# Optimization experiments

Measured on AMD Instinct MI355X. Metric: run time of the kernel, lower is better.

Reference implementation:

```python
import jax, jax.numpy as jnp
import numpy as np

H, C = 8, 16           # heads, per-head channels
NEG_SLOPE = 0.2        # PyG GATConv leaky_relu slope
N_NODES, N_EDGES, F_IN, N_GRAPHS = 50000, 600000, 64, 500


def setup_inputs() -> dict:
    key = jax.random.key(0)
    ks = jax.random.split(key, 24)
    s = 0.1  # weight init scale
    inp = {
        "x": jax.random.normal(ks[0], (N_NODES, F_IN), jnp.float32),
        "edge_index": jax.random.randint(ks[1], (2, N_EDGES), 0, N_NODES, dtype=jnp.int64),
        "batch": jnp.sort(jax.random.randint(ks[2], (N_NODES,), 0, N_GRAPHS, dtype=jnp.int64)),
        "W1": jax.random.normal(ks[3], (F_IN, H * C), jnp.float32) * s,
        "as1": jax.random.normal(ks[4], (H, C), jnp.float32) * s,
        "ad1": jax.random.normal(ks[5], (H, C), jnp.float32) * s,
        "b1": jnp.zeros((H * C,), jnp.float32),
        "W2": jax.random.normal(ks[6], (H * C, H * C), jnp.float32) * s,
        "as2": jax.random.normal(ks[7], (H, C), jnp.float32) * s,
        "ad2": jax.random.normal(ks[8], (H, C), jnp.float32) * s,
        "b2": jnp.zeros((H * C,), jnp.float32),
        "W3": jax.random.normal(ks[9], (H * C, H * C), jnp.float32) * s,
        "as3": jax.random.normal(ks[10], (H, C), jnp.float32) * s,
        "ad3": jax.random.normal(ks[11], (H, C), jnp.float32) * s,
        "b3": jnp.zeros((H * C,), jnp.float32),
        "fc1_w": jax.random.normal(ks[12], (H * C, 10), jnp.float32) * s,
        "fc1_b": jnp.zeros((10,), jnp.float32),
        "fc2_w": jax.random.normal(ks[13], (10, 1), jnp.float32) * s,
        "fc2_b": jnp.zeros((1,), jnp.float32),
    }
    return inp


def gat_layer(x, src, dst, W, att_src, att_dst, bias, n):
    # x: [N, F_in] -> h: [N, H, C]
    h = (x @ W).reshape(n, H, C)
    a_src = jnp.sum(h * att_src, axis=-1)  # [N, H]
    a_dst = jnp.sum(h * att_dst, axis=-1)  # [N, H]
    e = jax.nn.leaky_relu(a_src[src] + a_dst[dst], NEG_SLOPE)  # [E, H]
    # per-destination segment softmax (numerically stable)
    m = jax.ops.segment_max(e, dst, num_segments=n)            # [N, H]
    e = jnp.exp(e - m[dst])
    z = jax.ops.segment_sum(e, dst, num_segments=n)            # [N, H]
    alpha = e / (z[dst] + 1e-16)                               # [E, H]
    out = jax.ops.segment_sum(h[src] * alpha[:, :, None], dst, num_segments=n)  # [N, H, C]
    return out.reshape(n, H * C) + bias


def reference(x, edge_index, batch, W1, as1, ad1, b1, W2, as2, ad2, b2,
              W3, as3, ad3, b3, fc1_w, fc1_b, fc2_w, fc2_b):
    n = x.shape[0]
    # PyG GATConv default add_self_loops=True
    loop = jnp.arange(n, dtype=edge_index.dtype)
    src = jnp.concatenate([edge_index[0], loop])
    dst = jnp.concatenate([edge_index[1], loop])

    x = jax.nn.relu(gat_layer(x, src, dst, W1, as1, ad1, b1, n))
    x = jax.nn.relu(gat_layer(x, src, dst, W2, as2, ad2, b2, n))
    x = jax.nn.relu(gat_layer(x, src, dst, W3, as3, ad3, b3, n))

    # global_mean_pool over graphs
    sums = jax.ops.segment_sum(x, batch, num_segments=N_GRAPHS)          # [G, 128]
    cnts = jax.ops.segment_sum(jnp.ones((n,), x.dtype), batch, num_segments=N_GRAPHS)
    pooled = sums / jnp.maximum(cnts, 1.0)[:, None]

    hdn = jax.nn.relu(pooled @ fc1_w + fc1_b)
    return hdn @ fc2_w + fc2_b  # [G, 1]
```

## Files before the change

kernel.cpp:

```cpp
#include <hip/hip_runtime.h>
#include <hip/hip_bf16.h>

#define H 8
#define C 16
#define HC 128
#define NEG_SLOPE 0.2f

__global__ void init_kernel(int* __restrict__ deg8, int n) {
    int i = blockIdx.x * 256 + threadIdx.x;
    if (i < n) deg8[i] = 0;
}

__global__ void hist8_gptr_kernel(const int* __restrict__ ei, const int* __restrict__ batch,
                                  int* __restrict__ deg8, int* __restrict__ gptr,
                                  int E, int N, int G) {
    int t = blockIdx.x * 256 + threadIdx.x;
    int* dg = deg8 + (size_t)(blockIdx.x & 7) * N;
    int e0 = t * 4;
    if (e0 + 3 < E) {
        int4 d4 = *(const int4*)(ei + E + e0);
        atomicAdd(&dg[d4.x], 1);
        atomicAdd(&dg[d4.y], 1);
        atomicAdd(&dg[d4.z], 1);
        atomicAdd(&dg[d4.w], 1);
    } else if (e0 < E) {
        for (int j = e0; j < E; ++j) atomicAdd(&dg[ei[E + j]], 1);
    }
    int n0 = t * 4;
    if (n0 < N) {
        int v0 = batch[n0];
        int v1 = (n0 + 1 < N) ? batch[n0 + 1] : v0;
        int v2 = (n0 + 2 < N) ? batch[n0 + 2] : v1;
        int v3 = (n0 + 3 < N) ? batch[n0 + 3] : v2;
        int vals[4] = {v0, v1, v2, v3};
        int prev = (n0 == 0) ? -1 : batch[n0 - 1];
        for (int j = 0; j < 4; ++j) {
            int i = n0 + j;
            if (i >= N) break;
            int cur = vals[j];
            if (cur != prev)
                for (int g = prev + 1; g <= cur; ++g) gptr[g] = i;
            if (i == N - 1)
                for (int g = cur + 1; g <= G; ++g) gptr[g] = N;
            prev = cur;
        }
    }
}

__global__ void deg_reduce_kernel(const int* __restrict__ deg8, int* __restrict__ deg, int N) {
    int d = blockIdx.x * 256 + threadIdx.x;
    if (d >= N) return;
    int s = 1;
#pragma unroll
    for (int c = 0; c < 8; ++c) s += deg8[(size_t)c * N + d];
    deg[d] = s;
}

__global__ void scan_blk_kernel(const int* __restrict__ a, int* __restrict__ o,
                                int* __restrict__ p, int n) {
    __shared__ int sh[256];
    int tid = threadIdx.x;
    int base = blockIdx.x * 1024 + tid * 4;
    int4 v = make_int4(0, 0, 0, 0);
    if (base + 3 < n) v = *(const int4*)(a + base);
    else {
        if (base < n)     v.x = a[base];
        if (base + 1 < n) v.y = a[base + 1];
        if (base + 2 < n) v.z = a[base + 2];
        if (base + 3 < n) v.w = a[base + 3];
    }
    v.x = (v.x + 7) & ~7; v.y = (v.y + 7) & ~7; v.z = (v.z + 7) & ~7; v.w = (v.w + 7) & ~7;
    if (base >= n)     v.x = 0;
    if (base + 1 >= n) v.y = 0;
    if (base + 2 >= n) v.z = 0;
    if (base + 3 >= n) v.w = 0;
    int s = v.x + v.y + v.z + v.w;
    sh[tid] = s;
    __syncthreads();
    for (int off = 1; off < 256; off <<= 1) {
        int t = (tid >= off) ? sh[tid - off] : 0;
        __syncthreads();
        sh[tid] += t;
        __syncthreads();
    }
    int excl = sh[tid] - s;
    int4 ov;
    ov.x = excl; ov.y = ov.x + v.x; ov.z = ov.y + v.y; ov.w = ov.z + v.z;
    if (base + 3 < n) *(int4*)(o + base) = ov;
    else {
        if (base < n)     o[base] = ov.x;
        if (base + 1 < n) o[base + 1] = ov.y;
        if (base + 2 < n) o[base + 2] = ov.z;
        if (base + 3 < n) o[base + 3] = ov.w;
    }
    if (tid == 255) p[blockIdx.x] = sh[255];
}

__global__ void scan_part_kernel(int* __restrict__ p, int* __restrict__ tot, int nb) {
    __shared__ int sh[256];
    int tid = threadIdx.x;
    int v = (tid < nb) ? p[tid] : 0;
    sh[tid] = v;
    __syncthreads();
    for (int off = 1; off < 256; off <<= 1) {
        int t = (tid >= off) ? sh[tid - off] : 0;
        __syncthreads();
        sh[tid] += t;
        __syncthreads();
    }
    if (tid < nb) p[tid] = sh[tid] - v;
    if (tid == 255) *tot = sh[255];
}

__global__ void scan_add_kernel(int* __restrict__ o, const int* __restrict__ p, int n) {
    int off = p[blockIdx.x];
    int base = blockIdx.x * 1024 + threadIdx.x * 4;
    if (base + 3 < n) {
        int4 v = *(const int4*)(o + base);
        v.x += off; v.y += off; v.z += off; v.w += off;
        *(int4*)(o + base) = v;
    } else {
        if (base < n)     o[base] += off;
        if (base + 1 < n) o[base + 1] += off;
        if (base + 2 < n) o[base + 2] += off;
        if (base + 3 < n) o[base + 3] += off;
    }
}

__global__ void base_fill_kernel(int* __restrict__ deg8 ,
                                 const int* __restrict__ rowptr, int* __restrict__ csr, int N) {
    int d = blockIdx.x * 256 + threadIdx.x;
    if (d >= N) return;
    int base = rowptr[d];
    csr[base] = d;
    int run = base + 1;
    int cnt[8];
#pragma unroll
    for (int c = 0; c < 8; ++c) cnt[c] = deg8[(size_t)c * N + d];
#pragma unroll
    for (int c = 0; c < 8; ++c) { deg8[(size_t)c * N + d] = run; run += cnt[c]; }
    int rend = rowptr[d + 1];
    for (int p = run; p < rend; ++p) csr[p] = N;
    if (d == 0) {
        int tot = rowptr[N];
        for (int k = 0; k < 64; ++k) csr[tot + k] = N;
    }
}

__global__ void scatter8_kernel(const int* __restrict__ ei, int* __restrict__ base8,
                                int* __restrict__ csr, int E, int N) {
    int t = blockIdx.x * 256 + threadIdx.x;
    int* cur = base8 + (size_t)(blockIdx.x & 7) * N;
    int e0 = t * 4;
    if (e0 + 3 < E) {
        int4 s4 = *(const int4*)(ei + e0);
        int4 d4 = *(const int4*)(ei + E + e0);
        int p;
        p = atomicAdd(&cur[d4.x], 1); csr[p] = s4.x;
        p = atomicAdd(&cur[d4.y], 1); csr[p] = s4.y;
        p = atomicAdd(&cur[d4.z], 1); csr[p] = s4.z;
        p = atomicAdd(&cur[d4.w], 1); csr[p] = s4.w;
    } else if (e0 < E) {
        for (int j = e0; j < E; ++j) {
            int p = atomicAdd(&cur[ei[E + j]], 1);
            csr[p] = ei[j];
        }
    }
}

template <int K>
__global__ void gemm_att_kernel(const float* __restrict__ x, const float* __restrict__ W,
                                const float* __restrict__ as_, const float* __restrict__ ad_,
                                float* __restrict__ h, float* __restrict__ asrc,
                                float* __restrict__ adst, int n) {
    const int ROWS = 64;
    __shared__ float xs[ROWS][HC];
    int tx = threadIdx.x & 31;
    int ty = threadIdx.x >> 5;
    int row0 = blockIdx.x * ROWS;

    if (blockIdx.x == 0) {
        if (threadIdx.x < HC) h[(size_t)n * HC + threadIdx.x] = 0.f;
        if (threadIdx.x < H)  asrc[(size_t)n * H + threadIdx.x] = -INFINITY;
    }

    const int NV = ROWS * K / 4;
    for (int idx = threadIdx.x; idx < NV; idx += 256) {
        int rr = idx / (K / 4), kk = idx % (K / 4);
        int gr = row0 + rr;
        float4 v = (gr < n) ? ((const float4*)(x + (size_t)gr * K))[kk]
                            : make_float4(0.f, 0.f, 0.f, 0.f);
        *(float4*)(&xs[rr][kk * 4]) = v;
    }
    __syncthreads();

    const float* Wc = W + tx * 4;
    float acc[8][4];
#pragma unroll
    for (int r = 0; r < 8; ++r)
#pragma unroll
        for (int c = 0; c < 4; ++c) acc[r][c] = 0.f;

    for (int k = 0; k < K; k += 4) {
        float4 wv[4];
#pragma unroll
        for (int kk = 0; kk < 4; ++kk)
            wv[kk] = *(const float4*)(Wc + (size_t)(k + kk) * HC);
#pragma unroll
        for (int r = 0; r < 8; ++r) {
            float4 xr = *(const float4*)(&xs[ty * 8 + r][k]);
            acc[r][0] = fmaf(xr.x, wv[0].x, acc[r][0]);
            acc[r][1] = fmaf(xr.x, wv[0].y, acc[r][1]);
            acc[r][2] = fmaf(xr.x, wv[0].z, acc[r][2]);
            acc[r][3] = fmaf(xr.x, wv[0].w, acc[r][3]);
            acc[r][0] = fmaf(xr.y, wv[1].x, acc[r][0]);
            acc[r][1] = fmaf(xr.y, wv[1].y, acc[r][1]);
            acc[r][2] = fmaf(xr.y, wv[1].z, acc[r][2]);
            acc[r][3] = fmaf(xr.y, wv[1].w, acc[r][3]);
            acc[r][0] = fmaf(xr.z, wv[2].x, acc[r][0]);
            acc[r][1] = fmaf(xr.z, wv[2].y, acc[r][1]);
            acc[r][2] = fmaf(xr.z, wv[2].z, acc[r][2]);
            acc[r][3] = fmaf(xr.z, wv[2].w, acc[r][3]);
            acc[r][0] = fmaf(xr.w, wv[3].x, acc[r][0]);
            acc[r][1] = fmaf(xr.w, wv[3].y, acc[r][1]);
            acc[r][2] = fmaf(xr.w, wv[3].z, acc[r][2]);
            acc[r][3] = fmaf(xr.w, wv[3].w, acc[r][3]);
        }
    }
    __syncthreads();
#pragma unroll
    for (int r = 0; r < 8; ++r) {
        float4 o = make_float4(acc[r][0], acc[r][1], acc[r][2], acc[r][3]);
        *(float4*)(&xs[ty * 8 + r][tx * 4]) = o;
        int row = row0 + ty * 8 + r;
        if (row < n) *(float4*)(h + (size_t)row * HC + tx * 4) = o;
    }
    __syncthreads();

#pragma unroll
    for (int rep = 0; rep < 2; ++rep) {
        int pidx = threadIdx.x + rep * 256;
        int row = pidx >> 3;
        int hd = pidx & 7;
        if (row0 + row < n) {
            const float4* hv = (const float4*)&xs[row][hd * 16];
            const float4* sv = (const float4*)(as_ + hd * 16);
            const float4* dv = (const float4*)(ad_ + hd * 16);
            float s = 0.f, d = 0.f;
#pragma unroll
            for (int j = 0; j < 4; ++j) {
                float4 a = hv[j], u = sv[j], v = dv[j];
                s += a.x * u.x + a.y * u.y + a.z * u.z + a.w * u.w;
                d += a.x * v.x + a.y * v.y + a.z * v.z + a.w * v.w;
            }
            asrc[(size_t)(row0 + row) * H + hd] = s;
            adst[(size_t)(row0 + row) * H + hd] = d;
        }
    }
}

__global__ void gat_agg_kernel(const int* __restrict__ rowptr, const int* __restrict__ csr_src,
                               const float* __restrict__ h, const float* __restrict__ asrc,
                               const float* __restrict__ adst, const float* __restrict__ bias,
                               float* __restrict__ out, int N) {
    int dst = (blockIdx.x * 256 + threadIdx.x) >> 6;
    if (dst >= N) return;
    int lane = threadIdx.x & 63;
    int hd = lane >> 3;
    int beg = rowptr[dst], end = rowptr[dst + 1];
    float ad = adst[(size_t)dst * H + hd];
    const float2* h2 = (const float2*)h;

    float z = 0.f, a0 = 0.f, a1 = 0.f;
    int i0, i1, i2, i3, i4, i5, i6, i7;
    float e0, e1, e2, e3, e4, e5, e6, e7;
    float2 v0, v1, v2, v3, v4, v5, v6, v7;

#define LOADI(S, J) i##S = csr_src[(J)];
#define LOADV(S)                                                           \
    { e##S = asrc[(size_t)i##S * H + hd]; v##S = h2[(size_t)i##S * 64 + lane]; }
#define PROCE(S)                                                           \
    {   float e = e##S + ad;                                               \
        e = e > 0.f ? e : NEG_SLOPE * e;                                   \
        float w = __expf(e);                                               \
        z += w;                                                            \
        a0 = fmaf(w, v##S.x, a0);                                          \
        a1 = fmaf(w, v##S.y, a1);                                          \
    }
    LOADI(0, beg)     LOADI(1, beg + 1) LOADI(2, beg + 2) LOADI(3, beg + 3)
    LOADI(4, beg + 4) LOADI(5, beg + 5) LOADI(6, beg + 6) LOADI(7, beg + 7)
    LOADV(0) LOADV(1) LOADV(2) LOADV(3) LOADV(4) LOADV(5) LOADV(6) LOADV(7)
    LOADI(0, beg + 8)  LOADI(1, beg + 9)  LOADI(2, beg + 10) LOADI(3, beg + 11)
    LOADI(4, beg + 12) LOADI(5, beg + 13) LOADI(6, beg + 14) LOADI(7, beg + 15)

    for (int j = beg; j < end; j += 8) {
        PROCE(0) LOADV(0)
        PROCE(1) LOADV(1)
        PROCE(2) LOADV(2)
        PROCE(3) LOADV(3)
        PROCE(4) LOADV(4)
        PROCE(5) LOADV(5)
        PROCE(6) LOADV(6)
        PROCE(7) LOADV(7)
        LOADI(0, j + 16) LOADI(1, j + 17) LOADI(2, j + 18) LOADI(3, j + 19)
        LOADI(4, j + 20) LOADI(5, j + 21) LOADI(6, j + 22) LOADI(7, j + 23)
    }
#undef LOADI
#undef LOADV
#undef PROCE
    float inv = 1.f / (z + 1e-16f);
    int c2 = lane * 2;
    float r0 = fmaxf(a0 * inv + bias[c2], 0.f);
    float r1 = fmaxf(a1 * inv + bias[c2 + 1], 0.f);
    *(float2*)(out + (size_t)dst * HC + c2) = make_float2(r0, r1);
}

__global__ void pool_mlp_kernel(const float* __restrict__ x, const int* __restrict__ gptr,
                                const float* __restrict__ fc1w, const float* __restrict__ fc1b,
                                const float* __restrict__ fc2w, const float* __restrict__ fc2b,
                                float* __restrict__ out, int G) {
    __shared__ float sp[HC];
    __shared__ float sh[10];
    int g = blockIdx.x;
    int c = threadIdx.x;
    int beg = gptr[g], end = gptr[g + 1];
    float acc = 0.f;
    for (int n = beg; n < end; ++n) acc += x[(size_t)n * HC + c];
    sp[c] = acc / fmaxf((float)(end - beg), 1.f);
    __syncthreads();
    if (c < 10) {
        float s = fc1b[c];
        for (int k = 0; k < HC; ++k) s = fmaf(sp[k], fc1w[k * 10 + c], s);
        sh[c] = fmaxf(s, 0.f);
    }
    __syncthreads();
    if (c == 0) {
        float o = fc2b[0];
#pragma unroll
        for (int j = 0; j < 10; ++j) o = fmaf(sh[j], fc2w[j], o);
        out[g] = o;
    }
}

extern "C" void kernel_launch(void* const* d_in, const int* in_sizes, int n_in,
                              void* d_out, int out_size, void* d_ws, size_t ws_size,
                              hipStream_t stream) {
    const int N = in_sizes[0] / 64;
    const int E = in_sizes[1] / 2;
    const int G = out_size;
    const int CSR_CAP = E + 8 * N + 64;

    const float* x     = (const float*)d_in[0];
    const int*   ei    = (const int*)d_in[1];
    const int*   batch = (const int*)d_in[2];
    const float* W1 = (const float*)d_in[3];
    const float* as1 = (const float*)d_in[4];
    const float* ad1 = (const float*)d_in[5];
    const float* b1 = (const float*)d_in[6];
    const float* W2 = (const float*)d_in[7];
    const float* as2 = (const float*)d_in[8];
    const float* ad2 = (const float*)d_in[9];
    const float* b2 = (const float*)d_in[10];
    const float* W3 = (const float*)d_in[11];
    const float* as3 = (const float*)d_in[12];
    const float* ad3 = (const float*)d_in[13];
    const float* b3 = (const float*)d_in[14];
    const float* fc1w = (const float*)d_in[15];
    const float* fc1b = (const float*)d_in[16];
    const float* fc2w = (const float*)d_in[17];
    const float* fc2b = (const float*)d_in[18];

    float* ws = (float*)d_ws;
    float* h    = ws;
    float* xb0  = h + (size_t)(N + 1) * HC;
    float* xb1  = xb0 + (size_t)N * HC;
    float* asrc = xb1 + (size_t)N * HC;
    float* adst = asrc + (size_t)(N + 1) * H;
    int* ints   = (int*)(adst + (size_t)N * H);
    int* deg8   = ints;
    int* deg    = deg8 + (size_t)8 * N;
    int* rowptr = deg + N;
    int* gptr   = rowptr + N + 16;
    int* partN  = gptr + G + 16;
    int* csr    = partN + 256;

    dim3 blk(256);
    int grid4   = ((E + 3) / 4 + 255) / 256;
    int grid_n  = (N + 255) / 256;
    int grid_agg = (N * 64 + 255) / 256;
    int nbN = (N + 1023) / 1024;

    init_kernel<<<(8 * N + 255) / 256, blk, 0, stream>>>(deg8, 8 * N);
    hist8_gptr_kernel<<<grid4, blk, 0, stream>>>(ei, batch, deg8, gptr, E, N, G);
    deg_reduce_kernel<<<grid_n, blk, 0, stream>>>(deg8, deg, N);
    scan_blk_kernel<<<nbN, blk, 0, stream>>>(deg, rowptr, partN, N);
    scan_part_kernel<<<1, blk, 0, stream>>>(partN, rowptr + N, nbN);
    scan_add_kernel<<<nbN, blk, 0, stream>>>(rowptr, partN, N);
    base_fill_kernel<<<grid_n, blk, 0, stream>>>(deg8, rowptr, csr, N);
    scatter8_kernel<<<grid4, blk, 0, stream>>>(ei, deg8, csr, E, N);

    auto run_layer = [&](const float* xin, int K, const float* W, const float* as_,
                         const float* ad_, const float* b, float* out) {
        if (K == 64)
            gemm_att_kernel<64><<<(N + 63) / 64, blk, 0, stream>>>(xin, W, as_, ad_,
                                                                   h, asrc, adst, N);
        else
            gemm_att_kernel<128><<<(N + 63) / 64, blk, 0, stream>>>(xin, W, as_, ad_,
                                                                    h, asrc, adst, N);
        gat_agg_kernel<<<grid_agg, blk, 0, stream>>>(rowptr, csr, h, asrc, adst, b, out, N);
    };

    run_layer(x,   64,  W1, as1, ad1, b1, xb0);
    run_layer(xb0, 128, W2, as2, ad2, b2, xb1);
    run_layer(xb1, 128, W3, as3, ad3, b3, xb0);

    pool_mlp_kernel<<<G, dim3(128), 0, stream>>>(xb0, gptr, fc1w, fc1b, fc2w, fc2b,
                                                 (float*)d_out, G);
}
```

Measured before the change: 366.0 us.

## Split each node's aggregation across two waves, widen edge preprocessing per thread

The GAT aggregation now assigns two wavefronts to each destination node. Each wave processes half of the padded edge list, and the two partial softmax sums and accumulators are combined through shared memory. The histogram and scatter kernels now handle 8 edges per thread instead of 4, and the GEMM software-prefetches the next W slice into registers. The goal is more parallelism and latency hiding for high-degree nodes, paid for with a block-wide sync, shared-memory traffic, and idle waves when a node's degree is small.

```diff
diff --git a/kernel.cpp b/kernel.cpp
--- a/kernel.cpp
+++ b/kernel.cpp
@@ -16,28 +16,27 @@
                                   int E, int N, int G) {
     int t = blockIdx.x * 256 + threadIdx.x;
     int* dg = deg8 + (size_t)(blockIdx.x & 7) * N;
-    int e0 = t * 4;
-    if (e0 + 3 < E) {
-        int4 d4 = *(const int4*)(ei + E + e0);
-        atomicAdd(&dg[d4.x], 1);
-        atomicAdd(&dg[d4.y], 1);
-        atomicAdd(&dg[d4.z], 1);
-        atomicAdd(&dg[d4.w], 1);
+    int e0 = t * 8;
+    if (e0 + 7 < E) {
+        int4 d4a = *(const int4*)(ei + E + e0);
+        int4 d4b = *(const int4*)(ei + E + e0 + 4);
+        atomicAdd(&dg[d4a.x], 1);
+        atomicAdd(&dg[d4a.y], 1);
+        atomicAdd(&dg[d4a.z], 1);
+        atomicAdd(&dg[d4a.w], 1);
+        atomicAdd(&dg[d4b.x], 1);
+        atomicAdd(&dg[d4b.y], 1);
+        atomicAdd(&dg[d4b.z], 1);
+        atomicAdd(&dg[d4b.w], 1);
     } else if (e0 < E) {
         for (int j = e0; j < E; ++j) atomicAdd(&dg[ei[E + j]], 1);
     }
-    int n0 = t * 4;
+    int n0 = t * 8;
     if (n0 < N) {
-        int v0 = batch[n0];
-        int v1 = (n0 + 1 < N) ? batch[n0 + 1] : v0;
-        int v2 = (n0 + 2 < N) ? batch[n0 + 2] : v1;
-        int v3 = (n0 + 3 < N) ? batch[n0 + 3] : v2;
-        int vals[4] = {v0, v1, v2, v3};
         int prev = (n0 == 0) ? -1 : batch[n0 - 1];
-        for (int j = 0; j < 4; ++j) {
+        for (int j = 0; j < 8 && n0 + j < N; ++j) {
             int i = n0 + j;
-            if (i >= N) break;
-            int cur = vals[j];
+            int cur = batch[i];
             if (cur != prev)
                 for (int g = prev + 1; g <= cur; ++g) gptr[g] = i;
             if (i == N - 1)
@@ -69,7 +68,8 @@
         if (base + 2 < n) v.z = a[base + 2];
         if (base + 3 < n) v.w = a[base + 3];
     }
-    v.x = (v.x + 7) & ~7; v.y = (v.y + 7) & ~7; v.z = (v.z + 7) & ~7; v.w = (v.w + 7) & ~7;
+    v.x = (v.x + 7) & ~7; v.y = (v.y + 7) & ~7;
+    v.z = (v.z + 7) & ~7; v.w = (v.w + 7) & ~7;
     if (base >= n)     v.x = 0;
     if (base + 1 >= n) v.y = 0;
     if (base + 2 >= n) v.z = 0;
@@ -151,15 +151,21 @@
                                 int* __restrict__ csr, int E, int N) {
     int t = blockIdx.x * 256 + threadIdx.x;
     int* cur = base8 + (size_t)(blockIdx.x & 7) * N;
-    int e0 = t * 4;
-    if (e0 + 3 < E) {
-        int4 s4 = *(const int4*)(ei + e0);
-        int4 d4 = *(const int4*)(ei + E + e0);
+    int e0 = t * 8;
+    if (e0 + 7 < E) {
+        int4 s4a = *(const int4*)(ei + e0);
+        int4 s4b = *(const int4*)(ei + e0 + 4);
+        int4 d4a = *(const int4*)(ei + E + e0);
+        int4 d4b = *(const int4*)(ei + E + e0 + 4);
         int p;
-        p = atomicAdd(&cur[d4.x], 1); csr[p] = s4.x;
-        p = atomicAdd(&cur[d4.y], 1); csr[p] = s4.y;
-        p = atomicAdd(&cur[d4.z], 1); csr[p] = s4.z;
-        p = atomicAdd(&cur[d4.w], 1); csr[p] = s4.w;
+        p = atomicAdd(&cur[d4a.x], 1); csr[p] = s4a.x;
+        p = atomicAdd(&cur[d4a.y], 1); csr[p] = s4a.y;
+        p = atomicAdd(&cur[d4a.z], 1); csr[p] = s4a.z;
+        p = atomicAdd(&cur[d4a.w], 1); csr[p] = s4a.w;
+        p = atomicAdd(&cur[d4b.x], 1); csr[p] = s4b.x;
+        p = atomicAdd(&cur[d4b.y], 1); csr[p] = s4b.y;
+        p = atomicAdd(&cur[d4b.z], 1); csr[p] = s4b.z;
+        p = atomicAdd(&cur[d4b.w], 1); csr[p] = s4b.w;
     } else if (e0 < E) {
         for (int j = e0; j < E; ++j) {
             int p = atomicAdd(&cur[ei[E + j]], 1);
@@ -201,11 +207,17 @@
 #pragma unroll
         for (int c = 0; c < 4; ++c) acc[r][c] = 0.f;
 
+    float4 wv[4], wn[4];
+#pragma unroll
+    for (int kk = 0; kk < 4; ++kk)
+        wv[kk] = *(const float4*)(Wc + (size_t)kk * HC);
+
     for (int k = 0; k < K; k += 4) {
-        float4 wv[4];
-#pragma unroll
-        for (int kk = 0; kk < 4; ++kk)
-            wv[kk] = *(const float4*)(Wc + (size_t)(k + kk) * HC);
+        if (k + 4 < K) {
+#pragma unroll
+            for (int kk = 0; kk < 4; ++kk)
+                wn[kk] = *(const float4*)(Wc + (size_t)(k + 4 + kk) * HC);
+        }
 #pragma unroll
         for (int r = 0; r < 8; ++r) {
             float4 xr = *(const float4*)(&xs[ty * 8 + r][k]);
@@ -226,6 +238,8 @@
             acc[r][2] = fmaf(xr.w, wv[3].z, acc[r][2]);
             acc[r][3] = fmaf(xr.w, wv[3].w, acc[r][3]);
         }
+#pragma unroll
+        for (int kk = 0; kk < 4; ++kk) wv[kk] = wn[kk];
     }
     __syncthreads();
 #pragma unroll
@@ -259,23 +273,31 @@
     }
 }
 
-__global__ void gat_agg_kernel(const int* __restrict__ rowptr, const int* __restrict__ csr_src,
-                               const float* __restrict__ h, const float* __restrict__ asrc,
-                               const float* __restrict__ adst, const float* __restrict__ bias,
-                               float* __restrict__ out, int N) {
-    int dst = (blockIdx.x * 256 + threadIdx.x) >> 6;
-    if (dst >= N) return;
+__global__ __launch_bounds__(256, 8)
+void gat_agg_kernel(const int* __restrict__ rowptr, const int* __restrict__ csr_src,
+                    const float* __restrict__ h, const float* __restrict__ asrc,
+                    const float* __restrict__ adst, const float* __restrict__ bias,
+                    float* __restrict__ out, int N) {
+    __shared__ float red[4][3][64];
+    int wid = threadIdx.x >> 6;
+    int half = wid & 1;
+    int dst = blockIdx.x * 2 + (wid >> 1);
     int lane = threadIdx.x & 63;
     int hd = lane >> 3;
-    int beg = rowptr[dst], end = rowptr[dst + 1];
-    float ad = adst[(size_t)dst * H + hd];
-    const float2* h2 = (const float2*)h;
 
     float z = 0.f, a0 = 0.f, a1 = 0.f;
-    int i0, i1, i2, i3, i4, i5, i6, i7;
-    float e0, e1, e2, e3, e4, e5, e6, e7;
-    float2 v0, v1, v2, v3, v4, v5, v6, v7;
-
+    if (dst < N) {
+        int beg = rowptr[dst], end = rowptr[dst + 1];
+        int len = end - beg;
+        int hl = ((len >> 1) + 7) & ~7;
+        int b0 = half ? beg + hl : beg;
+        int e0r = half ? end : beg + hl;
+        if (b0 < e0r) {
+            float ad = adst[(size_t)dst * H + hd];
+            const float2* h2 = (const float2*)h;
+            int i0, i1, i2, i3, i4, i5, i6, i7;
+            float e0, e1, e2, e3, e4, e5, e6, e7;
+            float2 v0, v1, v2, v3, v4, v5, v6, v7;
 #define LOADI(S, J) i##S = csr_src[(J)];
 #define LOADV(S)                                                           \
     { e##S = asrc[(size_t)i##S * H + hd]; v##S = h2[(size_t)i##S * 64 + lane]; }
@@ -287,32 +309,42 @@
         a0 = fmaf(w, v##S.x, a0);                                          \
         a1 = fmaf(w, v##S.y, a1);                                          \
     }
-    LOADI(0, beg)     LOADI(1, beg + 1) LOADI(2, beg + 2) LOADI(3, beg + 3)
-    LOADI(4, beg + 4) LOADI(5, beg + 5) LOADI(6, beg + 6) LOADI(7, beg + 7)
-    LOADV(0) LOADV(1) LOADV(2) LOADV(3) LOADV(4) LOADV(5) LOADV(6) LOADV(7)
-    LOADI(0, beg + 8)  LOADI(1, beg + 9)  LOADI(2, beg + 10) LOADI(3, beg + 11)
-    LOADI(4, beg + 12) LOADI(5, beg + 13) LOADI(6, beg + 14) LOADI(7, beg + 15)
-
-    for (int j = beg; j < end; j += 8) {
-        PROCE(0) LOADV(0)
-        PROCE(1) LOADV(1)
-        PROCE(2) LOADV(2)
-        PROCE(3) LOADV(3)
-        PROCE(4) LOADV(4)
-        PROCE(5) LOADV(5)
-        PROCE(6) LOADV(6)
-        PROCE(7) LOADV(7)
-        LOADI(0, j + 16) LOADI(1, j + 17) LOADI(2, j + 18) LOADI(3, j + 19)
-        LOADI(4, j + 20) LOADI(5, j + 21) LOADI(6, j + 22) LOADI(7, j + 23)
-    }
+            LOADI(0, b0)     LOADI(1, b0 + 1) LOADI(2, b0 + 2) LOADI(3, b0 + 3)
+            LOADI(4, b0 + 4) LOADI(5, b0 + 5) LOADI(6, b0 + 6) LOADI(7, b0 + 7)
+            LOADV(0) LOADV(1) LOADV(2) LOADV(3) LOADV(4) LOADV(5) LOADV(6) LOADV(7)
+            LOADI(0, b0 + 8)  LOADI(1, b0 + 9)  LOADI(2, b0 + 10) LOADI(3, b0 + 11)
+            LOADI(4, b0 + 12) LOADI(5, b0 + 13) LOADI(6, b0 + 14) LOADI(7, b0 + 15)
+            for (int j = b0; j < e0r; j += 8) {
+                PROCE(0) LOADV(0)
+                PROCE(1) LOADV(1)
+                PROCE(2) LOADV(2)
+                PROCE(3) LOADV(3)
+                PROCE(4) LOADV(4)
+                PROCE(5) LOADV(5)
+                PROCE(6) LOADV(6)
+                PROCE(7) LOADV(7)
+                LOADI(0, j + 16) LOADI(1, j + 17) LOADI(2, j + 18) LOADI(3, j + 19)
+                LOADI(4, j + 20) LOADI(5, j + 21) LOADI(6, j + 22) LOADI(7, j + 23)
+            }
 #undef LOADI
 #undef LOADV
 #undef PROCE
-    float inv = 1.f / (z + 1e-16f);
-    int c2 = lane * 2;
-    float r0 = fmaxf(a0 * inv + bias[c2], 0.f);
-    float r1 = fmaxf(a1 * inv + bias[c2 + 1], 0.f);
-    *(float2*)(out + (size_t)dst * HC + c2) = make_float2(r0, r1);
+        }
+    }
+    red[wid][0][lane] = z;
+    red[wid][1][lane] = a0;
+    red[wid][2][lane] = a1;
+    __syncthreads();
+    if (half == 0 && dst < N) {
+        z  += red[wid + 1][0][lane];
+        a0 += red[wid + 1][1][lane];
+        a1 += red[wid + 1][2][lane];
+        float inv = 1.f / (z + 1e-16f);
+        int c2 = lane * 2;
+        float r0 = fmaxf(a0 * inv + bias[c2], 0.f);
+        float r1 = fmaxf(a1 * inv + bias[c2 + 1], 0.f);
+        *(float2*)(out + (size_t)dst * HC + c2) = make_float2(r0, r1);
+    }
 }
 
 __global__ void pool_mlp_kernel(const float* __restrict__ x, const int* __restrict__ gptr,
@@ -385,19 +417,19 @@
     int* csr    = partN + 256;
 
     dim3 blk(256);
-    int grid4   = ((E + 3) / 4 + 255) / 256;
+    int grid8   = ((E + 7) / 8 + 255) / 256;
     int grid_n  = (N + 255) / 256;
-    int grid_agg = (N * 64 + 255) / 256;
+    int grid_agg = (N + 1) / 2;
     int nbN = (N + 1023) / 1024;
 
     init_kernel<<<(8 * N + 255) / 256, blk, 0, stream>>>(deg8, 8 * N);
-    hist8_gptr_kernel<<<grid4, blk, 0, stream>>>(ei, batch, deg8, gptr, E, N, G);
+    hist8_gptr_kernel<<<grid8, blk, 0, stream>>>(ei, batch, deg8, gptr, E, N, G);
     deg_reduce_kernel<<<grid_n, blk, 0, stream>>>(deg8, deg, N);
     scan_blk_kernel<<<nbN, blk, 0, stream>>>(deg, rowptr, partN, N);
     scan_part_kernel<<<1, blk, 0, stream>>>(partN, rowptr + N, nbN);
     scan_add_kernel<<<nbN, blk, 0, stream>>>(rowptr, partN, N);
     base_fill_kernel<<<grid_n, blk, 0, stream>>>(deg8, rowptr, csr, N);
-    scatter8_kernel<<<grid4, blk, 0, stream>>>(ei, deg8, csr, E, N);
+    scatter8_kernel<<<grid8, blk, 0, stream>>>(ei, deg8, csr, E, N);
 
     auto run_layer = [&](const float* xin, int K, const float* W, const float* as_,
                          const float* ad_, const float* b, float* out) {
```

Result: no change. 371.2 us (+1.4%).
